# Performance work log

Measured on AMD Instinct MI355X. Metric: run time of the kernel, lower is better.

## Reference

```python
import jax, jax.numpy as jnp
import numpy as np

DIM = 1024
NUM_HEADS = 16
NUM_KV_HEADS = 4
HEAD_DIM = DIM // NUM_HEADS
KV_DIM = NUM_KV_HEADS * HEAD_DIM
PARTIAL_ROPE_DIM = 32
ROPE_BASE = 10000.0
LORA_RANK = 4
NUM_LORA_STEPS = 2
LORA_SCALE = 1.0
B, S = 2, 2048


def _rms_norm(x):
    eps = jnp.asarray(jnp.finfo(x.dtype).eps, x.dtype)
    return x * jax.lax.rsqrt(jnp.mean(x * x, axis=-1, keepdims=True) + eps)


def _rope_cos_sin(seq_len, dtype):
    half = PARTIAL_ROPE_DIM // 2
    inv_freq = 1.0 / (ROPE_BASE ** (jnp.arange(0, PARTIAL_ROPE_DIM, 2, dtype=jnp.float32) / PARTIAL_ROPE_DIM))
    t = jnp.arange(seq_len, dtype=jnp.float32)
    freqs = jnp.outer(t, inv_freq)  # [S, half]
    return jnp.cos(freqs).astype(dtype), jnp.sin(freqs).astype(dtype)


def _apply_rope_partial(x, cos, sin):
    # x: [B, H, S, D]; rotate first PARTIAL_ROPE_DIM dims, pass the rest.
    half = PARTIAL_ROPE_DIM // 2
    x1 = x[..., :half]
    x2 = x[..., half:PARTIAL_ROPE_DIM]
    xp = x[..., PARTIAL_ROPE_DIM:]
    c = cos[None, None, :, :]
    s = sin[None, None, :, :]
    return jnp.concatenate([x1 * c + x2 * s, -x1 * s + x2 * c, xp], axis=-1)


def setup_inputs() -> dict:
    key = jax.random.key(0)
    ks = jax.random.split(key, 12)
    std = 0.02
    return {
        "x": jax.random.normal(ks[0], (B, S, DIM), jnp.float32),
        "Wq": jax.random.normal(ks[1], (DIM, DIM), jnp.float32) * std,
        "Wk": jax.random.normal(ks[2], (KV_DIM, DIM), jnp.float32) * std,
        "Wv": jax.random.normal(ks[3], (KV_DIM, DIM), jnp.float32) * std,
        "Wproj": jax.random.normal(ks[4], (DIM, DIM), jnp.float32) * std,
        "q_gain": jnp.full((NUM_HEADS,), 1.0, jnp.float32),
        "lora_A_q": jax.random.normal(ks[5], (NUM_LORA_STEPS, LORA_RANK, DIM), jnp.float32) * std,
        "lora_B_q": jax.random.normal(ks[6], (NUM_LORA_STEPS, DIM, LORA_RANK), jnp.float32) * std,
        "lora_A_v": jax.random.normal(ks[7], (NUM_LORA_STEPS, LORA_RANK, DIM), jnp.float32) * std,
        "lora_B_v": jax.random.normal(ks[8], (NUM_LORA_STEPS, KV_DIM, LORA_RANK), jnp.float32) * std,
        "step_idx": 0,
    }


def reference(x, Wq, Wk, Wv, Wproj, q_gain, lora_A_q, lora_B_q, lora_A_v, lora_B_v, step_idx):
    bsz, seqlen, dim = x.shape
    q = x @ Wq.T
    v = x @ Wv.T
    if 0 <= step_idx < NUM_LORA_STEPS:
        q = q + LORA_SCALE * ((x @ lora_A_q[step_idx].T) @ lora_B_q[step_idx].T)
        v = v + LORA_SCALE * ((x @ lora_A_v[step_idx].T) @ lora_B_v[step_idx].T)
    k = x @ Wk.T

    q = q.reshape(bsz, seqlen, NUM_HEADS, HEAD_DIM).transpose(0, 2, 1, 3)      # [B,H,S,D]
    k = k.reshape(bsz, seqlen, NUM_KV_HEADS, HEAD_DIM).transpose(0, 2, 1, 3)   # [B,Hkv,S,D]
    v = v.reshape(bsz, seqlen, NUM_KV_HEADS, HEAD_DIM).transpose(0, 2, 1, 3)

    q = _rms_norm(q)
    k = _rms_norm(k)

    cos, sin = _rope_cos_sin(seqlen, q.dtype)
    q = _apply_rope_partial(q, cos, sin)
    k = _apply_rope_partial(k, cos, sin)

    q = q * q_gain.astype(q.dtype)[None, :, None, None]

    # GQA causal SDPA
    groups = NUM_HEADS // NUM_KV_HEADS
    qg = q.reshape(bsz, NUM_KV_HEADS, groups, seqlen, HEAD_DIM)
    scale = 1.0 / np.sqrt(HEAD_DIM)
    scores = jnp.einsum('bkgsd,bktd->bkgst', qg, k) * scale  # [B,Hkv,G,S,S]
    causal = jnp.tril(jnp.ones((seqlen, seqlen), bool))
    scores = jnp.where(causal[None, None, None], scores, jnp.asarray(-jnp.inf, scores.dtype))
    attn = jax.nn.softmax(scores, axis=-1)
    y = jnp.einsum('bkgst,bktd->bkgsd', attn, v)
    y = y.reshape(bsz, NUM_HEADS, seqlen, HEAD_DIM).transpose(0, 2, 1, 3).reshape(bsz, seqlen, dim)
    return y @ Wproj.T
```

## Files before the change

### kernel.cpp

```cpp
#include <hip/hip_runtime.h>
#include <hip/hip_bf16.h>
#include <stdint.h>

#define DIM 1024
#define NH 16
#define NKV 4
#define HD 64
#define SEQ 2048
#define BATCH 2
#define RANK 4
#define NSTEPS 2

#define XN      4194304
#define WQ_END  5242880
#define WK_END  5505024
#define WV_END  5767168
#define CVT_BLOCKS 6656
#define LORA_BLOCKS 1024

typedef unsigned short u16;
typedef unsigned int u32;
typedef __attribute__((ext_vector_type(8))) __bf16 bf16x8;
typedef __attribute__((ext_vector_type(4))) float f32x4;

__device__ __forceinline__ float bf2f(u16 v) {
    u32 u = ((u32)v) << 16;
    return __builtin_bit_cast(float, u);
}
__device__ __forceinline__ u16 f2bf(float f) {
    u32 u = __builtin_bit_cast(u32, f);
    u32 r = (u + 0x7fffu + ((u >> 16) & 1u)) >> 16;
    return (u16)r;
}
__device__ __forceinline__ u32 pk2(float a, float b) {
    return (u32)f2bf(a) | ((u32)f2bf(b) << 16);
}
__device__ __forceinline__ u32 pk2t(float a, float b) {
    return __builtin_amdgcn_perm(__builtin_bit_cast(u32, b),
                                 __builtin_bit_cast(u32, a), 0x07060302u);
}
__device__ __forceinline__ void glds16(const u16* g, u16* l) {
    __builtin_amdgcn_global_load_lds(
        (const __attribute__((address_space(1))) u32*)g,
        (__attribute__((address_space(3))) u32*)l, 16, 0, 0);
}

__global__ __launch_bounds__(256) void k_prep(
    const float* __restrict__ x, const float* __restrict__ Wq,
    const float* __restrict__ Wk, const float* __restrict__ Wv,
    const float* __restrict__ Wp, u16* __restrict__ dst,
    const float* __restrict__ Aq, const float* __restrict__ Av,
    const int* __restrict__ step_p, float* __restrict__ tq, float* __restrict__ tv)
{
    int bx = blockIdx.x;
    if (bx < CVT_BLOCKS) {
        int e = (bx * 256 + threadIdx.x) * 4;
        const float* src;
        if (e < XN)          src = x  + e;
        else if (e < WQ_END) src = Wq + (e - XN);
        else if (e < WK_END) src = Wk + (e - WQ_END);
        else if (e < WV_END) src = Wv + (e - WK_END);
        else                 src = Wp + (e - WV_END);
        float4 v = *(const float4*)src;
        *(uint2*)(dst + e) = make_uint2(pk2(v.x, v.y), pk2(v.z, v.w));
        return;
    }
    int wave = ((bx - CVT_BLOCKS) * 256 + threadIdx.x) >> 6;
    int lane = threadIdx.x & 63;
    int step = step_p[0];
    int valid = (step >= 0 && step < NSTEPS);
    int sc = valid ? step : 0;
    const float* xr = x + wave * DIM + lane * 16;
    float xf[16];
#pragma unroll
    for (int q = 0; q < 4; q++) {
        float4 v4 = *(const float4*)(xr + q * 4);
        xf[q * 4 + 0] = v4.x; xf[q * 4 + 1] = v4.y;
        xf[q * 4 + 2] = v4.z; xf[q * 4 + 3] = v4.w;
    }
    float sums[8];
#pragma unroll
    for (int j = 0; j < 8; j++) {
        const float* ar = (j < 4 ? Aq + sc * RANK * DIM + j * DIM
                                 : Av + sc * RANK * DIM + (j - 4) * DIM) + lane * 16;
        float s = 0.f;
#pragma unroll
        for (int q = 0; q < 4; q++) {
            float4 a4 = *(const float4*)(ar + q * 4);
            s += xf[q * 4 + 0] * a4.x + xf[q * 4 + 1] * a4.y
               + xf[q * 4 + 2] * a4.z + xf[q * 4 + 3] * a4.w;
        }
#pragma unroll
        for (int o = 32; o > 0; o >>= 1) s += __shfl_xor(s, o, 64);
        sums[j] = s;
    }
    if (!valid) {
#pragma unroll
        for (int j = 0; j < 8; j++) sums[j] = 0.f;
    }
    if (lane == 0) {
        tq[wave * 4 + 0] = sums[0]; tq[wave * 4 + 1] = sums[1];
        tq[wave * 4 + 2] = sums[2]; tq[wave * 4 + 3] = sums[3];
        tv[wave * 4 + 0] = sums[4]; tv[wave * 4 + 1] = sums[5];
        tv[wave * 4 + 2] = sums[6]; tv[wave * 4 + 3] = sums[7];
    }
}

__global__ __launch_bounds__(256) void k_gemm_qkv(
    const u16* __restrict__ A, const u16* __restrict__ B,
    u16* __restrict__ qkv, u16* __restrict__ vtb,
    const float* __restrict__ tq, const float* __restrict__ Bq,
    const float* __restrict__ tv, const float* __restrict__ Bv,
    const float* __restrict__ gain, const int* __restrict__ step_p)
{
    __shared__ __align__(16) u16 As[8192];
    __shared__ __align__(16) u16 Bs[8192];
    int bx = blockIdx.x;
    int xcd = bx & 7, o = bx >> 3;
    int bm = xcd * 4 + (o & 3);
    int bn = o >> 2;
    int t = threadIdx.x, lane = t & 63, w = t >> 6;
    int wy = w >> 1, wx = w & 1;
    int wb = t & ~63;
    int quad = lane >> 4, n16 = lane & 15;
    f32x4 acc[4][4];
#pragma unroll
    for (int i = 0; i < 4; i++)
#pragma unroll
        for (int j = 0; j < 4; j++) acc[i][j] = (f32x4){0.f, 0.f, 0.f, 0.f};

    int goff[4];
#pragma unroll
    for (int u = 0; u < 4; u++) {
        int idx = u * 256 + t;
        int grp = idx >> 6;
        int q_ = (idx >> 4) & 3, m = idx & 15;
        goff[u] = ((grp >> 1) * 16 + m) * DIM + (grp & 1) * 32 + q_ * 8;
    }
    const u16* Ab = A + bm * 128 * DIM;
    const u16* Bb = B + bn * 128 * DIM;

#pragma unroll 1
    for (int kb = 0; kb < 16; kb++) {
        int k0 = kb * 64;
        __syncthreads();
#pragma unroll
        for (int u = 0; u < 4; u++)
            glds16(Ab + goff[u] + k0, As + (u * 256 + wb) * 8);
#pragma unroll
        for (int u = 0; u < 4; u++)
            glds16(Bb + goff[u] + k0, Bs + (u * 256 + wb) * 8);
        __syncthreads();
#pragma unroll
        for (int c = 0; c < 2; c++) {
            bf16x8 af[4], bfr[4];
#pragma unroll
            for (int i = 0; i < 4; i++)
                af[i] = *(const bf16x8*)(As + (((wy * 4 + i) * 2 + c) * 64 + lane) * 8);
#pragma unroll
            for (int j = 0; j < 4; j++)
                bfr[j] = *(const bf16x8*)(Bs + (((wx * 4 + j) * 2 + c) * 64 + lane) * 8);
#pragma unroll
            for (int i = 0; i < 4; i++)
#pragma unroll
                for (int j = 0; j < 4; j++)
                    acc[i][j] = __builtin_amdgcn_mfma_f32_16x16x32_bf16(af[i], bfr[j], acc[i][j], 0, 0, 0);
        }
    }

    int step = step_p[0];
    int sc = (step >= 0 && step < NSTEPS) ? step : 0;
    int row_base = bm * 128 + wy * 64 + quad * 4;

    if (bn < 10) {
        bool isq = (bn < 8);
        int h2 = isq ? (bn * 2 + wx) : ((bn - 8) * 2 + wx);
        int colbase = isq ? (h2 * 64) : (1024 + h2 * 64);
        if (isq) {
            float4 B4[4];
#pragma unroll
            for (int j = 0; j < 4; j++)
                B4[j] = *(const float4*)(Bq + (sc * DIM + h2 * 64 + j * 16 + n16) * RANK);
#pragma unroll
            for (int i = 0; i < 4; i++)
#pragma unroll
                for (int r = 0; r < 4; r++) {
                    float4 t4 = *(const float4*)(tq + (row_base + i * 16 + r) * 4);
#pragma unroll
                    for (int j = 0; j < 4; j++)
                        acc[i][j][r] += t4.x * B4[j].x + t4.y * B4[j].y
                                      + t4.z * B4[j].z + t4.w * B4[j].w;
                }
        }
        float postmul = isq ? (gain[h2] * 0.125f * 1.4426950408889634f) : 1.f;
        float invf = exp2f(-(float)n16 * 0.8304820237218405f);
#pragma unroll
        for (int i = 0; i < 4; i++)
#pragma unroll
            for (int r = 0; r < 4; r++) {
                float s = acc[i][0][r] * acc[i][0][r] + acc[i][1][r] * acc[i][1][r]
                        + acc[i][2][r] * acc[i][2][r] + acc[i][3][r] * acc[i][3][r];
#pragma unroll
                for (int o2 = 1; o2 < 16; o2 <<= 1) s += __shfl_xor(s, o2, 64);
                float rr = rsqrtf(s * (1.f / 64.f) + 1.1920928955078125e-7f);
                int row = row_base + i * 16 + r;
                float v0 = acc[i][0][r] * rr, v1 = acc[i][1][r] * rr;
                float v2 = acc[i][2][r] * rr, v3 = acc[i][3][r] * rr;
                float ang = (float)(row & 2047) * invf;
                float cs = cosf(ang), sn = sinf(ang);
                float o0 = v0 * cs + v1 * sn;
                float o1 = -v0 * sn + v1 * cs;
                u16* dst = qkv + row * 1536 + colbase + n16;
                dst[0]  = f2bf(o0 * postmul);
                dst[16] = f2bf(o1 * postmul);
                dst[32] = f2bf(v2 * postmul);
                dst[48] = f2bf(v3 * postmul);
            }
    } else {
        int g = (bn - 10) * 2 + wx;
        float4 B4[4];
#pragma unroll
        for (int j = 0; j < 4; j++)
            B4[j] = *(const float4*)(Bv + (sc * (NKV * HD) + g * 64 + j * 16 + n16) * RANK);
#pragma unroll
        for (int i = 0; i < 4; i++) {
#pragma unroll
            for (int r = 0; r < 4; r++) {
                float4 t4 = *(const float4*)(tv + (row_base + i * 16 + r) * 4);
#pragma unroll
                for (int j = 0; j < 4; j++)
                    acc[i][j][r] += t4.x * B4[j].x + t4.y * B4[j].y
                                  + t4.z * B4[j].z + t4.w * B4[j].w;
            }
            int row0 = row_base + i * 16;
            int b = row0 >> 11, s0 = row0 & 2047;
#pragma unroll
            for (int j = 0; j < 4; j++) {
                int d = j * 16 + n16;
                uint2 pkv = make_uint2(pk2(acc[i][j][0], acc[i][j][1]),
                                       pk2(acc[i][j][2], acc[i][j][3]));
                *(uint2*)(vtb + ((b * NKV + g) * HD + d) * SEQ + s0) = pkv;
            }
        }
    }
}

__global__ __launch_bounds__(256) void k_gemm_proj(
    const u16* __restrict__ A, const u16* __restrict__ B,
    float* __restrict__ C)
{
    __shared__ __align__(16) u16 As[8192];
    __shared__ __align__(16) u16 Bs[4096];
    int bx = blockIdx.x;
    int bn = (bx & 7) * 2 + ((bx >> 3) & 1);
    int bm = bx >> 4;
    int t = threadIdx.x, lane = t & 63, w = t >> 6;
    int wy = w >> 1, wx = w & 1;
    int wb = t & ~63;
    f32x4 acc[4][2];
#pragma unroll
    for (int i = 0; i < 4; i++)
#pragma unroll
        for (int j = 0; j < 2; j++) acc[i][j] = (f32x4){0.f, 0.f, 0.f, 0.f};

    int goffA[4], goffB[2];
#pragma unroll
    for (int u = 0; u < 4; u++) {
        int idx = u * 256 + t;
        int grp = idx >> 6;
        int q_ = (idx >> 4) & 3, m = idx & 15;
        goffA[u] = ((grp >> 1) * 16 + m) * DIM + (grp & 1) * 32 + q_ * 8;
    }
#pragma unroll
    for (int u = 0; u < 2; u++) {
        int idx = u * 256 + t;
        int grp = idx >> 6;
        int q_ = (idx >> 4) & 3, m = idx & 15;
        goffB[u] = ((grp >> 1) * 16 + m) * DIM + (grp & 1) * 32 + q_ * 8;
    }
    const u16* Ab = A + bm * 128 * DIM;
    const u16* Bb = B + bn * 64 * DIM;

#pragma unroll 1
    for (int kb = 0; kb < 16; kb++) {
        int k0 = kb * 64;
        __syncthreads();
#pragma unroll
        for (int u = 0; u < 4; u++)
            glds16(Ab + goffA[u] + k0, As + (u * 256 + wb) * 8);
#pragma unroll
        for (int u = 0; u < 2; u++)
            glds16(Bb + goffB[u] + k0, Bs + (u * 256 + wb) * 8);
        __syncthreads();
#pragma unroll
        for (int c = 0; c < 2; c++) {
            bf16x8 af[4], bfr[2];
#pragma unroll
            for (int i = 0; i < 4; i++)
                af[i] = *(const bf16x8*)(As + (((wy * 4 + i) * 2 + c) * 64 + lane) * 8);
#pragma unroll
            for (int j = 0; j < 2; j++)
                bfr[j] = *(const bf16x8*)(Bs + (((wx * 2 + j) * 2 + c) * 64 + lane) * 8);
#pragma unroll
            for (int i = 0; i < 4; i++)
#pragma unroll
                for (int j = 0; j < 2; j++)
                    acc[i][j] = __builtin_amdgcn_mfma_f32_16x16x32_bf16(af[i], bfr[j], acc[i][j], 0, 0, 0);
        }
    }
    int quad = lane >> 4, n16 = lane & 15;
#pragma unroll
    for (int i = 0; i < 4; i++)
#pragma unroll
        for (int j = 0; j < 2; j++) {
            int col = bn * 64 + wx * 32 + j * 16 + n16;
#pragma unroll
            for (int r = 0; r < 4; r++) {
                int rowm = bm * 128 + wy * 64 + i * 16 + quad * 4 + r;
                C[rowm * DIM + col] = acc[i][j][r];
            }
        }
}

__global__ __launch_bounds__(256) void k_attn(
    const u16* __restrict__ qkv, const u16* __restrict__ vt,
    const float* __restrict__ gain, u16* __restrict__ y)
{
    __shared__ __align__(16) u16 kf[2][4096];
    __shared__ __align__(16) u16 vf[2][4096];
    __shared__ __align__(16) u16 pb[4][1024];
    int bx = blockIdx.x;
    int bgid = bx & 7, inner = bx >> 3;
    int b = bgid >> 2, g = bgid & 3;
    int h = g * 4 + (inner & 3);
    int qt = 31 - (inner >> 2);
    int t = threadIdx.x, lane = t & 63, w = t >> 6, wb = t & ~63;
    int quad = lane >> 4, n16 = lane & 15;
    float negM = -11.67f * fabsf(gain[h]);

    const u16* kbase = qkv + b * SEQ * 1536 + 1024 + g * HD;
    const u16* vbase = vt + (b * NKV + g) * HD * SEQ;

    int koff0, koff1, voff0, voff1;
    {
        int s0 = t, r0 = s0 >> 3, c0 = (s0 & 7) ^ (r0 & 7);
        koff0 = r0 * 1536 + c0 * 8;  voff0 = r0 * 2048 + c0 * 8;
        int s1 = 256 + t, r1 = s1 >> 3, c1 = (s1 & 7) ^ (r1 & 7);
        koff1 = r1 * 1536 + c1 * 8;  voff1 = r1 * 2048 + c1 * 8;
    }
    int swb = n16 & 7;
    int o0 = n16 * 8 + (quad ^ swb);
    int o1 = n16 * 8 + ((4 + quad) ^ swb);
    u16* pw = pb[w];

    f32x4 acc[4];
    float ps = 0.f;
#pragma unroll
    for (int i = 0; i < 4; i++) acc[i] = (f32x4){0.f, 0.f, 0.f, 0.f};
    int qrow = qt * 64 + w * 16 + n16;
    bf16x8 qlo, qhi;
    {
        const u16* qp = qkv + (b * SEQ + qrow) * 1536 + h * HD + quad * 8;
        qlo = *(const bf16x8*)qp;
        qhi = *(const bf16x8*)(qp + 32);
    }

    auto stage = [&](int kt, int p) {
        const u16* kp = kbase + kt * (64 * 1536);
        const u16* vp = vbase + kt * 64;
        glds16(kp + koff0, kf[p] + wb * 8);
        glds16(kp + koff1, kf[p] + (256 + wb) * 8);
        glds16(vp + voff0, vf[p] + wb * 8);
        glds16(vp + voff1, vf[p] + (256 + wb) * 8);
    };
    auto tilecomp = [&](int kt, int p, bool diag) {
        f32x4 st[4];
        __builtin_amdgcn_s_setprio(1);
#pragma unroll
        for (int nt = 0; nt < 4; nt++) {
            f32x4 sa = (f32x4){0.f, 0.f, 0.f, 0.f};
            sa = __builtin_amdgcn_mfma_f32_16x16x32_bf16(*(bf16x8*)(kf[p] + (nt * 128 + o0) * 8), qlo, sa, 0, 0, 0);
            sa = __builtin_amdgcn_mfma_f32_16x16x32_bf16(*(bf16x8*)(kf[p] + (nt * 128 + o1) * 8), qhi, sa, 0, 0, 0);
            st[nt] = sa;
        }
        __builtin_amdgcn_s_setprio(0);
        float pr[4][4];
        if (diag) {
            int kb0 = kt * 64;
#pragma unroll
            for (int nt = 0; nt < 4; nt++)
#pragma unroll
                for (int r = 0; r < 4; r++) {
                    int key = kb0 + nt * 16 + quad * 4 + r;
                    float e = exp2f(st[nt][r] + negM);
                    e = (key > qrow) ? 0.f : e;
                    pr[nt][r] = e;
                    ps += e;
                }
        } else {
#pragma unroll
            for (int nt = 0; nt < 4; nt++)
#pragma unroll
                for (int r = 0; r < 4; r++) {
                    float e = exp2f(st[nt][r] + negM);
                    pr[nt][r] = e;
                    ps += e;
                }
        }
#pragma unroll
        for (int nt = 0; nt < 4; nt++) {
            u32 lo = pk2t(pr[nt][0], pr[nt][1]);
            u32 hi = pk2t(pr[nt][2], pr[nt][3]);
            int ck = nt >> 1;
            int qbk = (nt & 1) * 2 + (quad >> 1);
            int byteoff = (ck * 64 + qbk * 16 + n16) * 16 + (quad & 1) * 8;
            *(uint2*)((char*)pw + byteoff) = make_uint2(lo, hi);
        }
        asm volatile("s_waitcnt lgkmcnt(0)" ::: "memory");
        __builtin_amdgcn_s_setprio(1);
#pragma unroll
        for (int ck = 0; ck < 2; ck++) {
            bf16x8 pfr = *(bf16x8*)(pw + (ck * 64 + lane) * 8);
            int oo = ck ? o1 : o0;
#pragma unroll
            for (int dt = 0; dt < 4; dt++)
                acc[dt] = __builtin_amdgcn_mfma_f32_16x16x32_bf16(*(bf16x8*)(vf[p] + (dt * 128 + oo) * 8), pfr, acc[dt], 0, 0, 0);
        }
        __builtin_amdgcn_s_setprio(0);
        asm volatile("" ::: "memory");
    };

    int ktEnd = qt + 1;
    int p = 0;
    stage(0, 0);
#pragma unroll 1
    for (int kt = 0; kt < ktEnd; kt++) {
        if (kt + 1 < ktEnd) {
            stage(kt + 1, p ^ 1);
            asm volatile("s_waitcnt vmcnt(4)" ::: "memory");
        } else {
            asm volatile("s_waitcnt vmcnt(0)" ::: "memory");
        }
        __builtin_amdgcn_s_barrier();
        tilecomp(kt, p, kt == ktEnd - 1);
        asm volatile("s_waitcnt lgkmcnt(0)" ::: "memory");
        __builtin_amdgcn_s_barrier();
        p ^= 1;
    }
    {
        float pt = ps + __shfl_xor(ps, 16, 64);
        pt += __shfl_xor(pt, 32, 64);
        float li = 1.f / pt;
#pragma unroll
        for (int dt = 0; dt < 4; dt++) {
            uint2 o = make_uint2(pk2(acc[dt][0] * li, acc[dt][1] * li),
                                 pk2(acc[dt][2] * li, acc[dt][3] * li));
            int d = dt * 16 + quad * 4;
            *(uint2*)(y + (b * SEQ + qrow) * DIM + h * HD + d) = o;
        }
    }
}

extern "C" void kernel_launch(void* const* d_in, const int* in_sizes, int n_in,
                              void* d_out, int out_size, void* d_ws, size_t ws_size,
                              hipStream_t stream)
{
    (void)in_sizes; (void)n_in; (void)out_size; (void)ws_size;
    const float* x     = (const float*)d_in[0];
    const float* Wq    = (const float*)d_in[1];
    const float* Wk    = (const float*)d_in[2];
    const float* Wv    = (const float*)d_in[3];
    const float* Wproj = (const float*)d_in[4];
    const float* qgain = (const float*)d_in[5];
    const float* Aq    = (const float*)d_in[6];
    const float* Bq    = (const float*)d_in[7];
    const float* Av    = (const float*)d_in[8];
    const float* Bv    = (const float*)d_in[9];
    const int*   step  = (const int*)d_in[10];

    char* ws = (char*)d_ws;
    u16* wsbf = (u16*)ws;
    u16* xb   = wsbf;
    u16* wf   = wsbf + XN;
    u16* wp   = wsbf + WV_END;
    u16* qkv  = (u16*)(ws + 13631488);
    float* tq = (float*)(ws + 26214400);
    float* tv = tq + 16384;
    u16* vt   = (u16*)(ws + 26607616);
    u16* y    = xb;

    k_prep<<<CVT_BLOCKS + LORA_BLOCKS, 256, 0, stream>>>(x, Wq, Wk, Wv, Wproj, wsbf,
                                                         Aq, Av, step, tq, tv);
    k_gemm_qkv<<<384, 256, 0, stream>>>(xb, wf, qkv, vt, tq, Bq, tv, Bv, qgain, step);
    k_attn<<<1024, 256, 0, stream>>>(qkv, vt, qgain, y);
    k_gemm_proj<<<512, 256, 0, stream>>>(y, wp, (float*)d_out);
}
```

Measured before the change: 207.1 us.

## Load K/V MFMA fragments directly from global memory, dropping LDS staging

The attention kernel stops double-buffering K and V tiles in shared memory through async global-to-LDS copies and barriers. Each wave now loads its K and V MFMA operand fragments straight from global memory into registers every tile. This removes the block-wide barriers and the LDS traffic, but all four waves now fetch the same K/V data redundantly through cache, and the loads are no longer prefetched ahead of compute, so memory latency is exposed unless the compiler overlaps it.

```diff
diff --git a/kernel.cpp b/kernel.cpp
--- a/kernel.cpp
+++ b/kernel.cpp
@@ -326,31 +326,18 @@
     const u16* __restrict__ qkv, const u16* __restrict__ vt,
     const float* __restrict__ gain, u16* __restrict__ y)
 {
-    __shared__ __align__(16) u16 kf[2][4096];
-    __shared__ __align__(16) u16 vf[2][4096];
     __shared__ __align__(16) u16 pb[4][1024];
     int bx = blockIdx.x;
     int bgid = bx & 7, inner = bx >> 3;
     int b = bgid >> 2, g = bgid & 3;
     int h = g * 4 + (inner & 3);
     int qt = 31 - (inner >> 2);
-    int t = threadIdx.x, lane = t & 63, w = t >> 6, wb = t & ~63;
+    int t = threadIdx.x, lane = t & 63, w = t >> 6;
     int quad = lane >> 4, n16 = lane & 15;
     float negM = -11.67f * fabsf(gain[h]);
 
-    const u16* kbase = qkv + b * SEQ * 1536 + 1024 + g * HD;
-    const u16* vbase = vt + (b * NKV + g) * HD * SEQ;
-
-    int koff0, koff1, voff0, voff1;
-    {
-        int s0 = t, r0 = s0 >> 3, c0 = (s0 & 7) ^ (r0 & 7);
-        koff0 = r0 * 1536 + c0 * 8;  voff0 = r0 * 2048 + c0 * 8;
-        int s1 = 256 + t, r1 = s1 >> 3, c1 = (s1 & 7) ^ (r1 & 7);
-        koff1 = r1 * 1536 + c1 * 8;  voff1 = r1 * 2048 + c1 * 8;
-    }
-    int swb = n16 & 7;
-    int o0 = n16 * 8 + (quad ^ swb);
-    int o1 = n16 * 8 + ((4 + quad) ^ swb);
+    const u16* kfr = qkv + b * SEQ * 1536 + 1024 + g * HD + n16 * 1536 + quad * 8;
+    const u16* vfr = vt + (b * NKV + g) * HD * SEQ + n16 * SEQ + quad * 8;
     u16* pw = pb[w];
 
     f32x4 acc[4];
@@ -365,22 +352,24 @@
         qhi = *(const bf16x8*)(qp + 32);
     }
 
-    auto stage = [&](int kt, int p) {
-        const u16* kp = kbase + kt * (64 * 1536);
-        const u16* vp = vbase + kt * 64;
-        glds16(kp + koff0, kf[p] + wb * 8);
-        glds16(kp + koff1, kf[p] + (256 + wb) * 8);
-        glds16(vp + voff0, vf[p] + wb * 8);
-        glds16(vp + voff1, vf[p] + (256 + wb) * 8);
-    };
-    auto tilecomp = [&](int kt, int p, bool diag) {
+    int ktEnd = qt + 1;
+#pragma unroll 1
+    for (int kt = 0; kt < ktEnd; kt++) {
+        bool diag = (kt == ktEnd - 1);
+        const u16* kb_ = kfr + kt * (64 * 1536);
+        bf16x8 ka[4][2];
+#pragma unroll
+        for (int nt = 0; nt < 4; nt++) {
+            ka[nt][0] = *(const bf16x8*)(kb_ + nt * 16 * 1536);
+            ka[nt][1] = *(const bf16x8*)(kb_ + nt * 16 * 1536 + 32);
+        }
         f32x4 st[4];
         __builtin_amdgcn_s_setprio(1);
 #pragma unroll
         for (int nt = 0; nt < 4; nt++) {
             f32x4 sa = (f32x4){0.f, 0.f, 0.f, 0.f};
-            sa = __builtin_amdgcn_mfma_f32_16x16x32_bf16(*(bf16x8*)(kf[p] + (nt * 128 + o0) * 8), qlo, sa, 0, 0, 0);
-            sa = __builtin_amdgcn_mfma_f32_16x16x32_bf16(*(bf16x8*)(kf[p] + (nt * 128 + o1) * 8), qhi, sa, 0, 0, 0);
+            sa = __builtin_amdgcn_mfma_f32_16x16x32_bf16(ka[nt][0], qlo, sa, 0, 0, 0);
+            sa = __builtin_amdgcn_mfma_f32_16x16x32_bf16(ka[nt][1], qhi, sa, 0, 0, 0);
             st[nt] = sa;
         }
         __builtin_amdgcn_s_setprio(0);
@@ -417,35 +406,19 @@
             *(uint2*)((char*)pw + byteoff) = make_uint2(lo, hi);
         }
         asm volatile("s_waitcnt lgkmcnt(0)" ::: "memory");
+        const u16* vb_ = vfr + kt * 64;
         __builtin_amdgcn_s_setprio(1);
 #pragma unroll
         for (int ck = 0; ck < 2; ck++) {
             bf16x8 pfr = *(bf16x8*)(pw + (ck * 64 + lane) * 8);
-            int oo = ck ? o1 : o0;
-#pragma unroll
-            for (int dt = 0; dt < 4; dt++)
-                acc[dt] = __builtin_amdgcn_mfma_f32_16x16x32_bf16(*(bf16x8*)(vf[p] + (dt * 128 + oo) * 8), pfr, acc[dt], 0, 0, 0);
+#pragma unroll
+            for (int dt = 0; dt < 4; dt++) {
+                bf16x8 va = *(const bf16x8*)(vb_ + dt * 16 * SEQ + ck * 32);
+                acc[dt] = __builtin_amdgcn_mfma_f32_16x16x32_bf16(va, pfr, acc[dt], 0, 0, 0);
+            }
         }
         __builtin_amdgcn_s_setprio(0);
         asm volatile("" ::: "memory");
-    };
-
-    int ktEnd = qt + 1;
-    int p = 0;
-    stage(0, 0);
-#pragma unroll 1
-    for (int kt = 0; kt < ktEnd; kt++) {
-        if (kt + 1 < ktEnd) {
-            stage(kt + 1, p ^ 1);
-            asm volatile("s_waitcnt vmcnt(4)" ::: "memory");
-        } else {
-            asm volatile("s_waitcnt vmcnt(0)" ::: "memory");
-        }
-        __builtin_amdgcn_s_barrier();
-        tilecomp(kt, p, kt == ktEnd - 1);
-        asm volatile("s_waitcnt lgkmcnt(0)" ::: "memory");
-        __builtin_amdgcn_s_barrier();
-        p ^= 1;
     }
     {
         float pt = ps + __shfl_xor(ps, 16, 64);
```

New measurement: 309.3 us. +49.4%, slower.
